# Kernel optimization log

Measured on AMD Instinct MI355X. Metric: run time of the kernel, lower is better.

Reference implementation:

```python
import jax, jax.numpy as jnp
import numpy as np

NEG_SLOPE = 0.01  # torch LeakyReLU default
MIN_FREQ = 1.0
MAX_FREQ = 10.0
W = 100
N_HIDDEN = 100
N_OBS = 64

def _leaky(x):
    return jnp.where(x >= 0, x, NEG_SLOPE * x)

def setup_inputs() -> dict:
    key = jax.random.key(0)
    ks = jax.random.split(key, 7)
    # kaiming_uniform-ish init scales (exact init doesn't matter for correctness baseline)
    def unif(k, shape, fan_in):
        bound = np.sqrt(6.0 / fan_in)
        return jax.random.uniform(k, shape, jnp.float32, -bound, bound)
    x = jax.random.normal(ks[0], (65536, N_OBS), jnp.float32)
    W_in = unif(ks[1], (N_OBS, W), N_OBS)
    b_in = jnp.zeros((W,), jnp.float32)
    Ws = unif(ks[2], (N_HIDDEN, W, W), W)
    bs = jnp.zeros((N_HIDDEN, W), jnp.float32)
    W_out = unif(ks[3], (W, 1), W)
    b_out = jnp.zeros((1,), jnp.float32)
    return {"x": x, "W_in": W_in, "b_in": b_in, "Ws": Ws, "bs": bs,
            "W_out": W_out, "b_out": b_out}

def reference(x, W_in, b_in, Ws, bs, W_out, b_out):
    h = _leaky(x @ W_in + b_in)                       # [B, 100]
    def layer(h, wb):
        w, b = wb
        return _leaky(h @ w + b), None
    h, _ = jax.lax.scan(layer, h, (Ws, bs))           # 100 hidden layers
    a = h @ W_out + b_out                             # [B, 1]
    a = jnp.tanh(a)
    return (a + 1.0) / 2.0 * (MAX_FREQ - MIN_FREQ) + MIN_FREQ
```

## Files before the change

kernel.cpp:

```cpp
#include <hip/hip_runtime.h>
#include <cmath>

#define NLAYERS 100
#define DIN     64
#define WDIM    100
#define NPAD    112
#define NT      7
#define ROWS    32
#define PSTR    136
#define PLANE   (16 * PSTR)

typedef _Float16 half8 __attribute__((ext_vector_type(8)));
typedef _Float16 half2v __attribute__((ext_vector_type(2)));
typedef __fp16   fp16x2 __attribute__((ext_vector_type(2)));
typedef float    f32x4 __attribute__((ext_vector_type(4)));

#define WSH_LAYER_HALVES (4 * NT * 64 * 8)
#define WSH_HALVES       (NLAYERS * WSH_LAYER_HALVES)
#define W0_HALVES        (2 * NT * 64 * 8)
#define BPAD_FLOATS      ((NLAYERS + 1) * NPAD)
#define OFF_BPAD_B       ((WSH_HALVES + W0_HALVES) * 2)
#define OFF_WOUT_B       (OFF_BPAD_B + BPAD_FLOATS * 4)
#define TOTAL_PREP       (WSH_HALVES + W0_HALVES + BPAD_FLOATS + NPAD)

__global__ void actor_prep(const float* __restrict__ Win, const float* __restrict__ bin,
                           const float* __restrict__ Ws,  const float* __restrict__ bs,
                           const float* __restrict__ Wout,
                           _Float16* __restrict__ wsh, _Float16* __restrict__ w0sh,
                           float* __restrict__ bpad, float* __restrict__ woutp) {
    int t = blockIdx.x * 256 + threadIdx.x;
    if (t < WSH_HALVES) {
        int j    = t & 7;
        int lane = (t >> 3) & 63;
        int fid  = t >> 9;
        int nt   = fid % 7;
        int r2   = fid / 7;
        int ks   = r2 & 3;
        int l    = r2 >> 2;
        int qq = lane >> 4, ll = lane & 15;
        int k = ks * 32 + qq * 8 + j;
        int n = nt * 16 + ll;
        float v = 0.f;
        if (k < WDIM && n < WDIM)       v = Ws[(l * WDIM + k) * WDIM + n];
        else if (k == 112 && n < WDIM)  v = bs[l * WDIM + n];
        wsh[t] = (_Float16)v;
        return;
    }
    int t2 = t - WSH_HALVES;
    if (t2 < W0_HALVES) {
        int j    = t2 & 7;
        int lane = (t2 >> 3) & 63;
        int fid  = t2 >> 9;
        int nt   = fid % 7;
        int ks   = fid / 7;
        int qq = lane >> 4, ll = lane & 15;
        int k = ks * 32 + qq * 8 + j;
        int n = nt * 16 + ll;
        float v = (k < DIN && n < WDIM) ? Win[k * WDIM + n] : 0.f;
        w0sh[t2] = (_Float16)v;
        return;
    }
    int t3 = t2 - W0_HALVES;
    if (t3 < BPAD_FLOATS) {
        int l = t3 / NPAD, c = t3 % NPAD;
        float v = 0.f;
        if (c < WDIM) v = (l == 0) ? bin[c] : bs[(l - 1) * WDIM + c];
        bpad[t3] = v;
        return;
    }
    int t4 = t3 - BPAD_FLOATS;
    if (t4 < NPAD) woutp[t4] = (t4 < WDIM) ? Wout[t4] : 0.f;
}

__device__ __forceinline__ void split8(const float* __restrict__ p, half8& hi, half8& lo) {
    f32x4 u0 = *(const f32x4*)p;
    f32x4 u1 = *(const f32x4*)(p + 4);
    float v[8] = {u0[0], u0[1], u0[2], u0[3], u1[0], u1[1], u1[2], u1[3]};
#pragma unroll
    for (int e = 0; e < 8; e += 2) {
        fp16x2 h = __builtin_amdgcn_cvt_pkrtz(v[e], v[e + 1]);
        float r0 = v[e]     - (float)h[0];
        float r1 = v[e + 1] - (float)h[1];
        fp16x2 l = __builtin_amdgcn_cvt_pkrtz(r0, r1);
        hi[e] = (_Float16)h[0]; hi[e + 1] = (_Float16)h[1];
        lo[e] = (_Float16)l[0]; lo[e + 1] = (_Float16)l[1];
    }
}

__device__ __forceinline__ void ep_tile(const f32x4 a, _Float16* __restrict__ d) {
    half2v p01, p23;
    p01[0] = (_Float16)a[0]; p01[1] = (_Float16)a[1];
    p23[0] = (_Float16)a[2]; p23[1] = (_Float16)a[3];
    const half2v slope = {(_Float16)0.01f, (_Float16)0.01f};
    p01 = __builtin_elementwise_max(p01, p01 * slope);
    p23 = __builtin_elementwise_max(p23, p23 * slope);
    uint2 w;
    w.x = __builtin_bit_cast(unsigned, p01);
    w.y = __builtin_bit_cast(unsigned, p23);
    *reinterpret_cast<uint2*>(d) = w;
}

__global__ __launch_bounds__(64, 2)
void actor_main(const float* __restrict__ x,
                const _Float16* __restrict__ wsh,
                const _Float16* __restrict__ w0sh,
                const float* __restrict__ bpad,
                const float* __restrict__ woutp,
                const float* __restrict__ bout,
                float* __restrict__ out) {
    __shared__ _Float16 hp[2 * PLANE];
    const int lane = threadIdx.x;
    const int q = lane >> 4, l15 = lane & 15;
    const int rowbase = blockIdx.x * ROWS;

    f32x4 acc0[NT], acc1[NT];
    half8 wb[4][NT];
    const f32x4 zero4 = {0.f, 0.f, 0.f, 0.f};

    {
        if (lane < 32) {
            const int pl = lane >> 4, row = lane & 15;
            const half8 z = {0, 0, 0, 0, 0, 0, 0, 0};
            *(half8*)(hp + pl * PLANE + row * PSTR + 112) = z;
            *(half8*)(hp + pl * PLANE + row * PSTR + 120) = z;
            hp[pl * PLANE + row * PSTR + 112] = (_Float16)1.0f;
        }
    }

#pragma unroll
    for (int ks = 0; ks < 2; ++ks)
#pragma unroll
        for (int nt = 0; nt < NT; ++nt)
            wb[ks][nt] = *(const half8*)(w0sh + (ks * 7 + nt) * 512 + lane * 8);
#pragma unroll
    for (int nt = 0; nt < NT; ++nt) {
        f32x4 b = *(const f32x4*)(bpad + nt * 16 + q * 4);
        acc0[nt] = b;
        acc1[nt] = b;
    }
#pragma unroll
    for (int ks = 0; ks < 2; ++ks) {
        half8 xhi, xlo;
        split8(x + (rowbase + l15) * DIN + ks * 32 + q * 8, xhi, xlo);
#pragma unroll
        for (int nt = 0; nt < NT; ++nt) {
            acc0[nt] = __builtin_amdgcn_mfma_f32_16x16x32_f16(wb[ks][nt], xhi, acc0[nt], 0, 0, 0);
            acc0[nt] = __builtin_amdgcn_mfma_f32_16x16x32_f16(wb[ks][nt], xlo, acc0[nt], 0, 0, 0);
        }
    }
#pragma unroll
    for (int ks = 0; ks < 2; ++ks) {
        half8 xhi, xlo;
        split8(x + (rowbase + 16 + l15) * DIN + ks * 32 + q * 8, xhi, xlo);
#pragma unroll
        for (int nt = 0; nt < NT; ++nt) {
            acc1[nt] = __builtin_amdgcn_mfma_f32_16x16x32_f16(wb[ks][nt], xhi, acc1[nt], 0, 0, 0);
            acc1[nt] = __builtin_amdgcn_mfma_f32_16x16x32_f16(wb[ks][nt], xlo, acc1[nt], 0, 0, 0);
        }
    }
#pragma unroll
    for (int ks = 0; ks < 4; ++ks) {
        const _Float16* wk = wsh + (ks * 7) * 512;
#pragma unroll
        for (int nt = 0; nt < NT; ++nt)
            wb[ks][nt] = *(const half8*)(wk + nt * 512 + lane * 8);
    }
#pragma unroll
    for (int nt = 0; nt < NT; ++nt)
        ep_tile(acc0[nt], hp + l15 * PSTR + nt * 16 + q * 4);

#pragma unroll 1
    for (int l = 0; l < NLAYERS; ++l) {
        const _Float16* wn = wsh + (l < NLAYERS - 1 ? l + 1 : l) * WSH_LAYER_HALVES;

        {
#pragma unroll
            for (int nt = 0; nt < NT; ++nt) acc0[nt] = zero4;
            _Float16* d1 = hp + PLANE + l15 * PSTR + q * 4;
#pragma unroll
            for (int ks = 0; ks < 4; ++ks) {
                half8 b0 = *(const half8*)(hp + l15 * PSTR + ks * 32 + q * 8);
#pragma unroll
                for (int nt = 0; nt < NT; ++nt)
                    acc0[nt] = __builtin_amdgcn_mfma_f32_16x16x32_f16(wb[ks][nt], b0, acc0[nt], 0, 0, 0);
                ep_tile(acc1[2 * ks], d1 + (2 * ks) * 16);
                if (ks < 3) ep_tile(acc1[2 * ks + 1], d1 + (2 * ks + 1) * 16);
            }
        }

        {
#pragma unroll
            for (int nt = 0; nt < NT; ++nt) acc1[nt] = zero4;
            _Float16* d0 = hp + l15 * PSTR + q * 4;
#pragma unroll
            for (int ks = 0; ks < 4; ++ks) {
                half8 b1 = *(const half8*)(hp + PLANE + l15 * PSTR + ks * 32 + q * 8);
#pragma unroll
                for (int nt = 0; nt < NT; ++nt)
                    acc1[nt] = __builtin_amdgcn_mfma_f32_16x16x32_f16(wb[ks][nt], b1, acc1[nt], 0, 0, 0);
                const _Float16* wk = wn + (ks * 7) * 512;
#pragma unroll
                for (int nt = 0; nt < NT; ++nt)
                    wb[ks][nt] = *(const half8*)(wk + nt * 512 + lane * 8);
                ep_tile(acc0[2 * ks], d0 + (2 * ks) * 16);
                if (ks < 3) ep_tile(acc0[2 * ks + 1], d0 + (2 * ks + 1) * 16);
            }
        }
    }

#pragma unroll
    for (int blk = 0; blk < 2; ++blk) {
        float s = 0.f;
#pragma unroll
        for (int nt = 0; nt < NT; ++nt) {
            f32x4 w4 = *(const f32x4*)(woutp + nt * 16 + q * 4);
            f32x4 a = blk ? acc1[nt] : acc0[nt];
#pragma unroll
            for (int r = 0; r < 4; ++r) {
                float v = fmaxf(a[r], 0.01f * a[r]);
                s += v * w4[r];
            }
        }
        s += __shfl_xor(s, 16);
        s += __shfl_xor(s, 32);
        if (q == 0) {
            float aa = s + bout[0];
            float t = tanhf(aa);
            out[rowbase + blk * 16 + l15] = t * 4.5f + 5.5f;
        }
    }
}

extern "C" void kernel_launch(void* const* d_in, const int* in_sizes, int n_in,
                              void* d_out, int out_size, void* d_ws, size_t ws_size,
                              hipStream_t stream) {
    const float* x    = (const float*)d_in[0];
    const float* Win  = (const float*)d_in[1];
    const float* bin  = (const float*)d_in[2];
    const float* Ws   = (const float*)d_in[3];
    const float* bs   = (const float*)d_in[4];
    const float* Wout = (const float*)d_in[5];
    const float* bout = (const float*)d_in[6];
    float* out = (float*)d_out;

    char* ws = (char*)d_ws;
    _Float16* wsh  = (_Float16*)ws;
    _Float16* w0sh = wsh + WSH_HALVES;
    float* bpad  = (float*)(ws + OFF_BPAD_B);
    float* woutp = (float*)(ws + OFF_WOUT_B);

    hipLaunchKernelGGL(actor_prep, dim3((TOTAL_PREP + 255) / 256), dim3(256), 0, stream,
                       Win, bin, Ws, bs, Wout, wsh, w0sh, bpad, woutp);

    const int nrows = in_sizes[0] / DIN;
    hipLaunchKernelGGL(actor_main, dim3(nrows / ROWS), dim3(64), 0, stream,
                       x, wsh, w0sh, bpad, woutp, bout, out);
}
```

Before: 271.8 us.

## Process three 16-row blocks per wavefront to reuse register-held weights

Each single-wavefront block now handles 48 rows instead of 32, adding a third accumulator set and LDS plane and rotating the software pipeline across three stages. Every weight fragment loaded into registers per layer now feeds three MFMA groups, which cuts weight traffic per row and gives more independent MFMA work to hide epilogue and LDS latency. In exchange it raises register and LDS pressure, which can lower occupancy, and the grid shrinks to about 1366 blocks with a partial tail block that is handled by clamping and bounds checks.

```diff
diff --git a/kernel.cpp b/kernel.cpp
--- a/kernel.cpp
+++ b/kernel.cpp
@@ -6,7 +6,7 @@
 #define WDIM    100
 #define NPAD    112
 #define NT      7
-#define ROWS    32
+#define ROWS    48
 #define PSTR    136
 #define PLANE   (16 * PSTR)
 
@@ -107,24 +107,22 @@
                 const float* __restrict__ bpad,
                 const float* __restrict__ woutp,
                 const float* __restrict__ bout,
-                float* __restrict__ out) {
-    __shared__ _Float16 hp[2 * PLANE];
+                float* __restrict__ out, int nrows) {
+    __shared__ _Float16 hp[3 * PLANE];
     const int lane = threadIdx.x;
     const int q = lane >> 4, l15 = lane & 15;
     const int rowbase = blockIdx.x * ROWS;
 
-    f32x4 acc0[NT], acc1[NT];
+    f32x4 acc0[NT], acc1[NT], acc2[NT];
     half8 wb[4][NT];
     const f32x4 zero4 = {0.f, 0.f, 0.f, 0.f};
 
-    {
-        if (lane < 32) {
-            const int pl = lane >> 4, row = lane & 15;
-            const half8 z = {0, 0, 0, 0, 0, 0, 0, 0};
-            *(half8*)(hp + pl * PLANE + row * PSTR + 112) = z;
-            *(half8*)(hp + pl * PLANE + row * PSTR + 120) = z;
-            hp[pl * PLANE + row * PSTR + 112] = (_Float16)1.0f;
-        }
+    if (lane < 48) {
+        const int pl = lane >> 4, row = lane & 15;
+        const half8 z = {0, 0, 0, 0, 0, 0, 0, 0};
+        *(half8*)(hp + pl * PLANE + row * PSTR + 112) = z;
+        *(half8*)(hp + pl * PLANE + row * PSTR + 120) = z;
+        hp[pl * PLANE + row * PSTR + 112] = (_Float16)1.0f;
     }
 
 #pragma unroll
@@ -135,27 +133,23 @@
 #pragma unroll
     for (int nt = 0; nt < NT; ++nt) {
         f32x4 b = *(const f32x4*)(bpad + nt * 16 + q * 4);
-        acc0[nt] = b;
-        acc1[nt] = b;
-    }
-#pragma unroll
-    for (int ks = 0; ks < 2; ++ks) {
-        half8 xhi, xlo;
-        split8(x + (rowbase + l15) * DIN + ks * 32 + q * 8, xhi, xlo);
-#pragma unroll
-        for (int nt = 0; nt < NT; ++nt) {
-            acc0[nt] = __builtin_amdgcn_mfma_f32_16x16x32_f16(wb[ks][nt], xhi, acc0[nt], 0, 0, 0);
-            acc0[nt] = __builtin_amdgcn_mfma_f32_16x16x32_f16(wb[ks][nt], xlo, acc0[nt], 0, 0, 0);
-        }
-    }
-#pragma unroll
-    for (int ks = 0; ks < 2; ++ks) {
-        half8 xhi, xlo;
-        split8(x + (rowbase + 16 + l15) * DIN + ks * 32 + q * 8, xhi, xlo);
-#pragma unroll
-        for (int nt = 0; nt < NT; ++nt) {
-            acc1[nt] = __builtin_amdgcn_mfma_f32_16x16x32_f16(wb[ks][nt], xhi, acc1[nt], 0, 0, 0);
-            acc1[nt] = __builtin_amdgcn_mfma_f32_16x16x32_f16(wb[ks][nt], xlo, acc1[nt], 0, 0, 0);
+        acc0[nt] = b; acc1[nt] = b; acc2[nt] = b;
+    }
+#pragma unroll
+    for (int blk = 0; blk < 3; ++blk) {
+        int row = rowbase + blk * 16 + l15;
+        if (row > nrows - 1) row = nrows - 1;
+        const float* xr = x + (long)row * DIN;
+#pragma unroll
+        for (int ks = 0; ks < 2; ++ks) {
+            half8 xhi, xlo;
+            split8(xr + ks * 32 + q * 8, xhi, xlo);
+            f32x4* a = (blk == 0) ? acc0 : (blk == 1) ? acc1 : acc2;
+#pragma unroll
+            for (int nt = 0; nt < NT; ++nt) {
+                a[nt] = __builtin_amdgcn_mfma_f32_16x16x32_f16(wb[ks][nt], xhi, a[nt], 0, 0, 0);
+                a[nt] = __builtin_amdgcn_mfma_f32_16x16x32_f16(wb[ks][nt], xlo, a[nt], 0, 0, 0);
+            }
         }
     }
 #pragma unroll
@@ -187,17 +181,30 @@
                 if (ks < 3) ep_tile(acc1[2 * ks + 1], d1 + (2 * ks + 1) * 16);
             }
         }
-
         {
 #pragma unroll
             for (int nt = 0; nt < NT; ++nt) acc1[nt] = zero4;
-            _Float16* d0 = hp + l15 * PSTR + q * 4;
+            _Float16* d2 = hp + 2 * PLANE + l15 * PSTR + q * 4;
 #pragma unroll
             for (int ks = 0; ks < 4; ++ks) {
                 half8 b1 = *(const half8*)(hp + PLANE + l15 * PSTR + ks * 32 + q * 8);
 #pragma unroll
                 for (int nt = 0; nt < NT; ++nt)
                     acc1[nt] = __builtin_amdgcn_mfma_f32_16x16x32_f16(wb[ks][nt], b1, acc1[nt], 0, 0, 0);
+                ep_tile(acc2[2 * ks], d2 + (2 * ks) * 16);
+                if (ks < 3) ep_tile(acc2[2 * ks + 1], d2 + (2 * ks + 1) * 16);
+            }
+        }
+        {
+#pragma unroll
+            for (int nt = 0; nt < NT; ++nt) acc2[nt] = zero4;
+            _Float16* d0 = hp + l15 * PSTR + q * 4;
+#pragma unroll
+            for (int ks = 0; ks < 4; ++ks) {
+                half8 b2 = *(const half8*)(hp + 2 * PLANE + l15 * PSTR + ks * 32 + q * 8);
+#pragma unroll
+                for (int nt = 0; nt < NT; ++nt)
+                    acc2[nt] = __builtin_amdgcn_mfma_f32_16x16x32_f16(wb[ks][nt], b2, acc2[nt], 0, 0, 0);
                 const _Float16* wk = wn + (ks * 7) * 512;
 #pragma unroll
                 for (int nt = 0; nt < NT; ++nt)
@@ -209,24 +216,25 @@
     }
 
 #pragma unroll
-    for (int blk = 0; blk < 2; ++blk) {
+    for (int blk = 0; blk < 3; ++blk) {
+        const f32x4* a = (blk == 0) ? acc0 : (blk == 1) ? acc1 : acc2;
         float s = 0.f;
 #pragma unroll
         for (int nt = 0; nt < NT; ++nt) {
             f32x4 w4 = *(const f32x4*)(woutp + nt * 16 + q * 4);
-            f32x4 a = blk ? acc1[nt] : acc0[nt];
 #pragma unroll
             for (int r = 0; r < 4; ++r) {
-                float v = fmaxf(a[r], 0.01f * a[r]);
+                float v = fmaxf(a[nt][r], 0.01f * a[nt][r]);
                 s += v * w4[r];
             }
         }
         s += __shfl_xor(s, 16);
         s += __shfl_xor(s, 32);
-        if (q == 0) {
+        const int row = rowbase + blk * 16 + l15;
+        if (q == 0 && row < nrows) {
             float aa = s + bout[0];
             float t = tanhf(aa);
-            out[rowbase + blk * 16 + l15] = t * 4.5f + 5.5f;
+            out[row] = t * 4.5f + 5.5f;
         }
     }
 }
@@ -253,6 +261,7 @@
                        Win, bin, Ws, bs, Wout, wsh, w0sh, bpad, woutp);
 
     const int nrows = in_sizes[0] / DIN;
-    hipLaunchKernelGGL(actor_main, dim3(nrows / ROWS), dim3(64), 0, stream,
-                       x, wsh, w0sh, bpad, woutp, bout, out);
-}
+    const int grid = (nrows + ROWS - 1) / ROWS;
+    hipLaunchKernelGGL(actor_main, dim3(grid), dim3(64), 0, stream,
+                       x, wsh, w0sh, bpad, woutp, bout, out, nrows);
+}
```

After: 286.6 us. 5.5% more time.

## Split output columns across two waves and process 64 rows per block

Applied to the files above, without the earlier changes.

Each block now has two wavefronts that split the padded output columns (8 tiles of 16, 4 per wave) and covers 64 rows as four 16-row tiles. Each per-lane weight fragment is reused across more rows, which roughly halves weight-fragment traffic per row. Layers are double-buffered in LDS with a barrier per layer. The bias is now folded in through a constant-one column that the padded weights propagate from layer to layer. The costs are a padded eighth column tile (more MFMA work), a block barrier every layer, and a cross-wave LDS reduction for the output head.

```diff
diff --git a/kernel.cpp b/kernel.cpp
--- a/kernel.cpp
+++ b/kernel.cpp
@@ -4,24 +4,27 @@
 #define NLAYERS 100
 #define DIN     64
 #define WDIM    100
-#define NPAD    112
-#define NT      7
-#define ROWS    32
+#define NTT     8
+#define NTW     4
+#define RT      4
+#define ROWS    64
 #define PSTR    136
-#define PLANE   (16 * PSTR)
+#define RTPLANE (16 * PSTR)
+#define BUF     (RT * RTPLANE)
 
 typedef _Float16 half8 __attribute__((ext_vector_type(8)));
 typedef _Float16 half2v __attribute__((ext_vector_type(2)));
 typedef __fp16   fp16x2 __attribute__((ext_vector_type(2)));
 typedef float    f32x4 __attribute__((ext_vector_type(4)));
 
-#define WSH_LAYER_HALVES (4 * NT * 64 * 8)
+#define WSH_LAYER_HALVES (4 * NTT * 64 * 8)
 #define WSH_HALVES       (NLAYERS * WSH_LAYER_HALVES)
-#define W0_HALVES        (2 * NT * 64 * 8)
-#define BPAD_FLOATS      ((NLAYERS + 1) * NPAD)
+#define W0_HALVES        (2 * NTT * 64 * 8)
+#define BPAD_FLOATS      128
 #define OFF_BPAD_B       ((WSH_HALVES + W0_HALVES) * 2)
 #define OFF_WOUT_B       (OFF_BPAD_B + BPAD_FLOATS * 4)
-#define TOTAL_PREP       (WSH_HALVES + W0_HALVES + BPAD_FLOATS + NPAD)
+#define WOUT_FLOATS      128
+#define TOTAL_PREP       (WSH_HALVES + W0_HALVES + BPAD_FLOATS + WOUT_FLOATS)
 
 __global__ void actor_prep(const float* __restrict__ Win, const float* __restrict__ bin,
                            const float* __restrict__ Ws,  const float* __restrict__ bs,
@@ -33,16 +36,16 @@
         int j    = t & 7;
         int lane = (t >> 3) & 63;
         int fid  = t >> 9;
-        int nt   = fid % 7;
-        int r2   = fid / 7;
+        int nt   = fid & 7;
+        int r2   = fid >> 3;
         int ks   = r2 & 3;
         int l    = r2 >> 2;
-        int qq = lane >> 4, ll = lane & 15;
-        int k = ks * 32 + qq * 8 + j;
-        int n = nt * 16 + ll;
+        int k = ks * 32 + (lane >> 4) * 8 + j;
+        int n = nt * 16 + (lane & 15);
         float v = 0.f;
-        if (k < WDIM && n < WDIM)       v = Ws[(l * WDIM + k) * WDIM + n];
-        else if (k == 112 && n < WDIM)  v = bs[l * WDIM + n];
+        if (k < WDIM && n < WDIM)            v = Ws[(l * WDIM + k) * WDIM + n];
+        else if (k == 112 && n < WDIM)       v = bs[l * WDIM + n];
+        else if (k == 112 && n == 112)       v = 1.0f;
         wsh[t] = (_Float16)v;
         return;
     }
@@ -51,25 +54,22 @@
         int j    = t2 & 7;
         int lane = (t2 >> 3) & 63;
         int fid  = t2 >> 9;
-        int nt   = fid % 7;
-        int ks   = fid / 7;
-        int qq = lane >> 4, ll = lane & 15;
-        int k = ks * 32 + qq * 8 + j;
-        int n = nt * 16 + ll;
+        int nt   = fid & 7;
+        int ks   = fid >> 3;
+        int k = ks * 32 + (lane >> 4) * 8 + j;
+        int n = nt * 16 + (lane & 15);
         float v = (k < DIN && n < WDIM) ? Win[k * WDIM + n] : 0.f;
         w0sh[t2] = (_Float16)v;
         return;
     }
     int t3 = t2 - W0_HALVES;
     if (t3 < BPAD_FLOATS) {
-        int l = t3 / NPAD, c = t3 % NPAD;
-        float v = 0.f;
-        if (c < WDIM) v = (l == 0) ? bin[c] : bs[(l - 1) * WDIM + c];
+        float v = (t3 < WDIM) ? bin[t3] : (t3 == 112 ? 1.0f : 0.f);
         bpad[t3] = v;
         return;
     }
     int t4 = t3 - BPAD_FLOATS;
-    if (t4 < NPAD) woutp[t4] = (t4 < WDIM) ? Wout[t4] : 0.f;
+    if (t4 < WOUT_FLOATS) woutp[t4] = (t4 < WDIM) ? Wout[t4] : 0.f;
 }
 
 __device__ __forceinline__ void split8(const float* __restrict__ p, half8& hi, half8& lo) {
@@ -100,7 +100,7 @@
     *reinterpret_cast<uint2*>(d) = w;
 }
 
-__global__ __launch_bounds__(64, 2)
+__global__ __launch_bounds__(128, 2)
 void actor_main(const float* __restrict__ x,
                 const _Float16* __restrict__ wsh,
                 const _Float16* __restrict__ w0sh,
@@ -108,125 +108,116 @@
                 const float* __restrict__ woutp,
                 const float* __restrict__ bout,
                 float* __restrict__ out) {
-    __shared__ _Float16 hp[2 * PLANE];
-    const int lane = threadIdx.x;
+    __shared__ _Float16 hp[2 * BUF];
+    const int lane = threadIdx.x & 63;
+    const int wid  = threadIdx.x >> 6;
     const int q = lane >> 4, l15 = lane & 15;
     const int rowbase = blockIdx.x * ROWS;
-
-    f32x4 acc0[NT], acc1[NT];
-    half8 wb[4][NT];
+    const int ntb = wid * NTW;
+
+    f32x4 acc[RT][NTW];
+    half8 wb[4][NTW];
     const f32x4 zero4 = {0.f, 0.f, 0.f, 0.f};
 
-    {
-        if (lane < 32) {
-            const int pl = lane >> 4, row = lane & 15;
-            const half8 z = {0, 0, 0, 0, 0, 0, 0, 0};
-            *(half8*)(hp + pl * PLANE + row * PSTR + 112) = z;
-            *(half8*)(hp + pl * PLANE + row * PSTR + 120) = z;
-            hp[pl * PLANE + row * PSTR + 112] = (_Float16)1.0f;
-        }
-    }
-
 #pragma unroll
     for (int ks = 0; ks < 2; ++ks)
 #pragma unroll
-        for (int nt = 0; nt < NT; ++nt)
-            wb[ks][nt] = *(const half8*)(w0sh + (ks * 7 + nt) * 512 + lane * 8);
-#pragma unroll
-    for (int nt = 0; nt < NT; ++nt) {
-        f32x4 b = *(const f32x4*)(bpad + nt * 16 + q * 4);
-        acc0[nt] = b;
-        acc1[nt] = b;
-    }
-#pragma unroll
-    for (int ks = 0; ks < 2; ++ks) {
-        half8 xhi, xlo;
-        split8(x + (rowbase + l15) * DIN + ks * 32 + q * 8, xhi, xlo);
-#pragma unroll
-        for (int nt = 0; nt < NT; ++nt) {
-            acc0[nt] = __builtin_amdgcn_mfma_f32_16x16x32_f16(wb[ks][nt], xhi, acc0[nt], 0, 0, 0);
-            acc0[nt] = __builtin_amdgcn_mfma_f32_16x16x32_f16(wb[ks][nt], xlo, acc0[nt], 0, 0, 0);
-        }
-    }
-#pragma unroll
-    for (int ks = 0; ks < 2; ++ks) {
-        half8 xhi, xlo;
-        split8(x + (rowbase + 16 + l15) * DIN + ks * 32 + q * 8, xhi, xlo);
-#pragma unroll
-        for (int nt = 0; nt < NT; ++nt) {
-            acc1[nt] = __builtin_amdgcn_mfma_f32_16x16x32_f16(wb[ks][nt], xhi, acc1[nt], 0, 0, 0);
-            acc1[nt] = __builtin_amdgcn_mfma_f32_16x16x32_f16(wb[ks][nt], xlo, acc1[nt], 0, 0, 0);
-        }
-    }
-#pragma unroll
-    for (int ks = 0; ks < 4; ++ks) {
-        const _Float16* wk = wsh + (ks * 7) * 512;
-#pragma unroll
-        for (int nt = 0; nt < NT; ++nt)
-            wb[ks][nt] = *(const half8*)(wk + nt * 512 + lane * 8);
-    }
-#pragma unroll
-    for (int nt = 0; nt < NT; ++nt)
-        ep_tile(acc0[nt], hp + l15 * PSTR + nt * 16 + q * 4);
+        for (int ntl = 0; ntl < NTW; ++ntl)
+            wb[ks][ntl] = *(const half8*)(w0sh + (ks * NTT + ntb + ntl) * 512 + lane * 8);
+#pragma unroll
+    for (int rt = 0; rt < RT; ++rt)
+#pragma unroll
+        for (int ntl = 0; ntl < NTW; ++ntl)
+            acc[rt][ntl] = *(const f32x4*)(bpad + (ntb + ntl) * 16 + q * 4);
+#pragma unroll
+    for (int rt = 0; rt < RT; ++rt) {
+        const float* xr = x + (rowbase + rt * 16 + l15) * DIN;
+#pragma unroll
+        for (int ks = 0; ks < 2; ++ks) {
+            half8 xhi, xlo;
+            split8(xr + ks * 32 + q * 8, xhi, xlo);
+#pragma unroll
+            for (int ntl = 0; ntl < NTW; ++ntl) {
+                acc[rt][ntl] = __builtin_amdgcn_mfma_f32_16x16x32_f16(wb[ks][ntl], xhi, acc[rt][ntl], 0, 0, 0);
+                acc[rt][ntl] = __builtin_amdgcn_mfma_f32_16x16x32_f16(wb[ks][ntl], xlo, acc[rt][ntl], 0, 0, 0);
+            }
+        }
+    }
+#pragma unroll
+    for (int rt = 0; rt < RT; ++rt)
+#pragma unroll
+        for (int ntl = 0; ntl < NTW; ++ntl)
+            ep_tile(acc[rt][ntl], hp + rt * RTPLANE + l15 * PSTR + (ntb + ntl) * 16 + q * 4);
+#pragma unroll
+    for (int ks = 0; ks < 4; ++ks)
+#pragma unroll
+        for (int ntl = 0; ntl < NTW; ++ntl)
+            wb[ks][ntl] = *(const half8*)(wsh + (ks * NTT + ntb + ntl) * 512 + lane * 8);
+    __syncthreads();
 
 #pragma unroll 1
     for (int l = 0; l < NLAYERS; ++l) {
+        const _Float16* rb = hp + (l & 1) * BUF;
+        _Float16* wbf = hp + ((l + 1) & 1) * BUF;
         const _Float16* wn = wsh + (l < NLAYERS - 1 ? l + 1 : l) * WSH_LAYER_HALVES;
 
-        {
-#pragma unroll
-            for (int nt = 0; nt < NT; ++nt) acc0[nt] = zero4;
-            _Float16* d1 = hp + PLANE + l15 * PSTR + q * 4;
+#pragma unroll
+        for (int rt = 0; rt < RT; ++rt) {
+            half8 bh[4];
+#pragma unroll
+            for (int ks = 0; ks < 4; ++ks)
+                bh[ks] = *(const half8*)(rb + rt * RTPLANE + l15 * PSTR + ks * 32 + q * 8);
+            _Float16* dprev = wbf + (rt - 1) * RTPLANE + l15 * PSTR + q * 4;
 #pragma unroll
             for (int ks = 0; ks < 4; ++ks) {
-                half8 b0 = *(const half8*)(hp + l15 * PSTR + ks * 32 + q * 8);
-#pragma unroll
-                for (int nt = 0; nt < NT; ++nt)
-                    acc0[nt] = __builtin_amdgcn_mfma_f32_16x16x32_f16(wb[ks][nt], b0, acc0[nt], 0, 0, 0);
-                ep_tile(acc1[2 * ks], d1 + (2 * ks) * 16);
-                if (ks < 3) ep_tile(acc1[2 * ks + 1], d1 + (2 * ks + 1) * 16);
+#pragma unroll
+                for (int ntl = 0; ntl < NTW; ++ntl)
+                    acc[rt][ntl] = __builtin_amdgcn_mfma_f32_16x16x32_f16(
+                        wb[ks][ntl], bh[ks], (ks == 0 ? zero4 : acc[rt][ntl]), 0, 0, 0);
+                if (rt >= 1)
+                    ep_tile(acc[rt - 1][ks], dprev + (ntb + ks) * 16);
+                if (rt == RT - 1) {
+#pragma unroll
+                    for (int ntl = 0; ntl < NTW; ++ntl)
+                        wb[ks][ntl] = *(const half8*)(wn + (ks * NTT + ntb + ntl) * 512 + lane * 8);
+                }
             }
         }
-
-        {
-#pragma unroll
-            for (int nt = 0; nt < NT; ++nt) acc1[nt] = zero4;
-            _Float16* d0 = hp + l15 * PSTR + q * 4;
-#pragma unroll
-            for (int ks = 0; ks < 4; ++ks) {
-                half8 b1 = *(const half8*)(hp + PLANE + l15 * PSTR + ks * 32 + q * 8);
-#pragma unroll
-                for (int nt = 0; nt < NT; ++nt)
-                    acc1[nt] = __builtin_amdgcn_mfma_f32_16x16x32_f16(wb[ks][nt], b1, acc1[nt], 0, 0, 0);
-                const _Float16* wk = wn + (ks * 7) * 512;
-#pragma unroll
-                for (int nt = 0; nt < NT; ++nt)
-                    wb[ks][nt] = *(const half8*)(wk + nt * 512 + lane * 8);
-                ep_tile(acc0[2 * ks], d0 + (2 * ks) * 16);
-                if (ks < 3) ep_tile(acc0[2 * ks + 1], d0 + (2 * ks + 1) * 16);
-            }
-        }
-    }
-
-#pragma unroll
-    for (int blk = 0; blk < 2; ++blk) {
+        _Float16* dlast = wbf + (RT - 1) * RTPLANE + l15 * PSTR + q * 4;
+#pragma unroll
+        for (int ntl = 0; ntl < NTW; ++ntl)
+            ep_tile(acc[RT - 1][ntl], dlast + (ntb + ntl) * 16);
+        __syncthreads();
+    }
+
+    float part[RT];
+#pragma unroll
+    for (int rt = 0; rt < RT; ++rt) {
         float s = 0.f;
 #pragma unroll
-        for (int nt = 0; nt < NT; ++nt) {
-            f32x4 w4 = *(const f32x4*)(woutp + nt * 16 + q * 4);
-            f32x4 a = blk ? acc1[nt] : acc0[nt];
+        for (int ntl = 0; ntl < NTW; ++ntl) {
+            f32x4 w4 = *(const f32x4*)(woutp + (ntb + ntl) * 16 + q * 4);
 #pragma unroll
             for (int r = 0; r < 4; ++r) {
-                float v = fmaxf(a[r], 0.01f * a[r]);
+                float a = acc[rt][ntl][r];
+                float v = fmaxf(a, 0.01f * a);
                 s += v * w4[r];
             }
         }
         s += __shfl_xor(s, 16);
         s += __shfl_xor(s, 32);
-        if (q == 0) {
-            float aa = s + bout[0];
-            float t = tanhf(aa);
-            out[rowbase + blk * 16 + l15] = t * 4.5f + 5.5f;
+        part[rt] = s;
+    }
+    float* red = (float*)hp;
+#pragma unroll
+    for (int rt = 0; rt < RT; ++rt)
+        if (q == 0) red[wid * 64 + rt * 16 + l15] = part[rt];
+    __syncthreads();
+    {
+        const int r = threadIdx.x;
+        if (r < 64) {
+            float tot = red[r] + red[64 + r] + bout[0];
+            out[rowbase + r] = tanhf(tot) * 4.5f + 5.5f;
         }
     }
 }
@@ -253,6 +244,6 @@
                        Win, bin, Ws, bs, Wout, wsh, w0sh, bpad, woutp);
 
     const int nrows = in_sizes[0] / DIN;
-    hipLaunchKernelGGL(actor_main, dim3(nrows / ROWS), dim3(64), 0, stream,
+    hipLaunchKernelGGL(actor_main, dim3(nrows / ROWS), dim3(128), 0, stream,
                        x, wsh, w0sh, bpad, woutp, bout, out);
 }
```

New measurement: 262.9 us. 3.3% less time.
